# Optimization experiments

Hardware: AMD Instinct MI355X
Metric: run time of the kernel (lower is better)

## Reference

```python
import jax, jax.numpy as jnp
import numpy as np

N, IN, H, C, HID, OUT, E = 4096, 28, 8, 256, 256, 128, 131072
NEG_SLOPE = 0.2


def _gat(x, src, dst, eattr, W, a_src, a_dst, W_e, a_edge, bias, concat):
    # PyG GATConv with edge_dim: add self-loops (edge_attr fill = mean),
    # per-edge attention logits, scatter-softmax over destination nodes.
    n = x.shape[0]
    loop = jnp.arange(n, dtype=src.dtype)
    src = jnp.concatenate([src, loop])
    dst = jnp.concatenate([dst, loop])
    mean_attr = jnp.broadcast_to(eattr.mean(axis=0, keepdims=True), (n, eattr.shape[1]))
    eattr = jnp.concatenate([eattr, mean_attr], axis=0)
    xp = (x @ W).reshape(n, H, C)                       # (N,H,C)
    a_s = (xp * a_src).sum(-1)                          # (N,H)
    a_d = (xp * a_dst).sum(-1)                          # (N,H)
    ep = (eattr @ W_e).reshape(-1, H, C)                # (E',H,C)
    a_e = (ep * a_edge).sum(-1)                         # (E',H)
    alpha = jax.nn.leaky_relu(a_s[src] + a_d[dst] + a_e, negative_slope=NEG_SLOPE)
    mx = jax.ops.segment_max(alpha, dst, num_segments=n)
    ex = jnp.exp(alpha - mx[dst])
    den = jax.ops.segment_sum(ex, dst, num_segments=n)
    w = ex / (den[dst] + 1e-16)                         # (E',H)
    out = jax.ops.segment_sum(xp[src] * w[:, :, None], dst, num_segments=n)  # (N,H,C)
    out = out.reshape(n, H * C) if concat else out.mean(axis=1)
    return out + bias


def _lstm_step(x, W_ih, W_hh, b_ih, b_hh):
    # single-timestep LSTM, zero initial (h, c); torch gate order i,f,g,o
    g = x @ W_ih.T + b_ih + b_hh
    i, f, gg, o = jnp.split(g, 4, axis=-1)
    c = jax.nn.sigmoid(i) * jnp.tanh(gg)
    return jax.nn.sigmoid(o) * jnp.tanh(c)


def _mha(x, in_w, in_b, out_w, out_b, nh):
    n, e = x.shape
    hd = e // nh
    qkv = x @ in_w.T + in_b
    q, k, v = jnp.split(qkv, 3, axis=-1)
    q = q.reshape(n, nh, hd).transpose(1, 0, 2)
    k = k.reshape(n, nh, hd).transpose(1, 0, 2)
    v = v.reshape(n, nh, hd).transpose(1, 0, 2)
    scale = jnp.asarray(1.0 / np.sqrt(hd), x.dtype)
    s = jnp.einsum('hnd,hmd->hnm', q, k) * scale
    p = jax.nn.softmax(s, axis=-1)
    o = jnp.einsum('hnm,hmd->hnd', p, v).transpose(1, 0, 2).reshape(n, e)
    return o @ out_w.T + out_b


def _forward(x, ei_t, ei_c, ea_t, ea_c,
             W_t, a_src_t, a_dst_t, We_t, a_edge_t, b_t,
             W_c, a_src_c, a_dst_c, We_c, a_edge_c, b_c,
             lstm_Wih, lstm_Whh, lstm_bih, lstm_bhh,
             mha_in_w, mha_in_b, mha_out_w, mha_out_b,
             fus_w, fus_b, out_w, out_b):
    # temporal branch: GAT (concat heads) -> 1-step LSTM
    h_t = _gat(x, ei_t[0], ei_t[1], ea_t, W_t, a_src_t, a_dst_t, We_t, a_edge_t, b_t, True)
    h_temporal = _lstm_step(h_t, lstm_Wih, lstm_Whh, lstm_bih, lstm_bhh)   # (N,HID)
    # causal branch: GAT (mean heads -> HID) -> full self-attention over nodes
    h_c = _gat(x, ei_c[0], ei_c[1], ea_c, W_c, a_src_c, a_dst_c, We_c, a_edge_c, b_c, False)
    h_causal = _mha(h_c, mha_in_w, mha_in_b, mha_out_w, mha_out_b, 4)      # (N,HID)
    h = jnp.concatenate([h_temporal, h_causal], axis=-1)
    h = jax.nn.relu(h @ fus_w.T + fus_b)
    out = h @ out_w.T + out_b
    return out, h_temporal, h_causal


def setup_inputs() -> dict:
    key = jax.random.key(0)
    ks = jax.random.split(key, 32)
    s = 0.05
    d = {
        'x': jax.random.normal(ks[0], (N, IN), jnp.float32),
        'edge_index_temporal': jax.random.randint(ks[1], (2, E), 0, N, jnp.int32),
        'edge_index_causal': jax.random.randint(ks[2], (2, E), 0, N, jnp.int32),
        'edge_attr_temporal': jax.random.uniform(ks[3], (E, 1), jnp.float32),
        'edge_attr_causal': jax.random.uniform(ks[4], (E, 1), jnp.float32),
        'W_t': jax.random.normal(ks[5], (IN, H * C), jnp.float32) * s,
        'a_src_t': jax.random.normal(ks[6], (H, C), jnp.float32) * s,
        'a_dst_t': jax.random.normal(ks[7], (H, C), jnp.float32) * s,
        'We_t': jax.random.normal(ks[8], (1, H * C), jnp.float32) * s,
        'a_edge_t': jax.random.normal(ks[9], (H, C), jnp.float32) * s,
        'b_t': jnp.zeros((H * C,), jnp.float32),
        'W_c': jax.random.normal(ks[10], (IN, H * C), jnp.float32) * s,
        'a_src_c': jax.random.normal(ks[11], (H, C), jnp.float32) * s,
        'a_dst_c': jax.random.normal(ks[12], (H, C), jnp.float32) * s,
        'We_c': jax.random.normal(ks[13], (1, H * C), jnp.float32) * s,
        'a_edge_c': jax.random.normal(ks[14], (H, C), jnp.float32) * s,
        'b_c': jnp.zeros((C,), jnp.float32),
        'lstm_Wih': jax.random.normal(ks[15], (4 * HID, H * C), jnp.float32) * s,
        'lstm_Whh': jax.random.normal(ks[16], (4 * HID, HID), jnp.float32) * s,
        'lstm_bih': jnp.zeros((4 * HID,), jnp.float32),
        'lstm_bhh': jnp.zeros((4 * HID,), jnp.float32),
        'mha_in_w': jax.random.normal(ks[17], (3 * HID, HID), jnp.float32) * s,
        'mha_in_b': jnp.zeros((3 * HID,), jnp.float32),
        'mha_out_w': jax.random.normal(ks[18], (HID, HID), jnp.float32) * s,
        'mha_out_b': jnp.zeros((HID,), jnp.float32),
        'fus_w': jax.random.normal(ks[19], (HID, 2 * HID), jnp.float32) * s,
        'fus_b': jnp.zeros((HID,), jnp.float32),
        'out_w': jax.random.normal(ks[20], (OUT, HID), jnp.float32) * s,
        'out_b': jnp.zeros((OUT,), jnp.float32),
    }
    return d


def reference(x, edge_index_temporal, edge_index_causal, edge_attr_temporal, edge_attr_causal,
              W_t, a_src_t, a_dst_t, We_t, a_edge_t, b_t,
              W_c, a_src_c, a_dst_c, We_c, a_edge_c, b_c,
              lstm_Wih, lstm_Whh, lstm_bih, lstm_bhh,
              mha_in_w, mha_in_b, mha_out_w, mha_out_b,
              fus_w, fus_b, out_w, out_b):
    return _forward(x, edge_index_temporal, edge_index_causal, edge_attr_temporal, edge_attr_causal,
                    W_t, a_src_t, a_dst_t, We_t, a_edge_t, b_t,
                    W_c, a_src_c, a_dst_c, We_c, a_edge_c, b_c,
                    lstm_Wih, lstm_Whh, lstm_bih, lstm_bhh,
                    mha_in_w, mha_in_b, mha_out_w, mha_out_b,
                    fus_w, fus_b, out_w, out_b)
```

## Files before the change

kernel.cpp:

```cpp
#include <hip/hip_runtime.h>
#include <hip/hip_bf16.h>

constexpr int NN_ = 4096;
constexpr int INF = 28;
constexpr int NH  = 8;
constexpr int CC  = 256;
constexpr int HC  = 2048;
constexpr int HID = 256;
constexpr int NE  = 131072;
constexpr int KK  = NH * INF;

typedef short bf16x8 __attribute__((ext_vector_type(8)));
typedef short bf16x4 __attribute__((ext_vector_type(4)));
typedef float f32x4 __attribute__((ext_vector_type(4)));

__device__ inline void split_store(float v, __hip_bfloat16* H, __hip_bfloat16* L, size_t idx)
{
    __hip_bfloat16 h = __float2bfloat16(v);
    H[idx] = h;
    L[idx] = __float2bfloat16(v - __bfloat162float(h));
}

__device__ inline short f2bs(float v)
{
    __hip_bfloat16 h = __float2bfloat16(v);
    return *reinterpret_cast<short*>(&h);
}

__device__ inline float wave_sum(float v)
{
    v += __shfl_xor(v, 1);  v += __shfl_xor(v, 2);  v += __shfl_xor(v, 4);
    v += __shfl_xor(v, 8);  v += __shfl_xor(v, 16); v += __shfl_xor(v, 32);
    return v;
}

__global__ void k_stage1(
    const float* __restrict__ Wih,  __hip_bfloat16* WihH,  __hip_bfloat16* WihL,
    const float* __restrict__ Wt,   __hip_bfloat16* WtH,   __hip_bfloat16* WtL,
    const float* __restrict__ minw, __hip_bfloat16* minH,  __hip_bfloat16* minL,
    const float* __restrict__ moutw,__hip_bfloat16* moutH, __hip_bfloat16* moutL,
    const float* __restrict__ fusw, __hip_bfloat16* fusH,  __hip_bfloat16* fusL,
    const float* __restrict__ outw, __hip_bfloat16* outH,  __hip_bfloat16* outL,
    const float* __restrict__ Wc,   __hip_bfloat16* BH,    __hip_bfloat16* BL,
    const float* __restrict__ ast, const float* __restrict__ adt,
    const float* __restrict__ Wet, const float* __restrict__ aet,
    const float* __restrict__ asc, const float* __restrict__ adc,
    const float* __restrict__ Wec, const float* __restrict__ aec,
    float* __restrict__ wa, float* __restrict__ dote,
    const float* __restrict__ bt, const float* __restrict__ bih, const float* __restrict__ bhh,
    float* __restrict__ bg,
    const float* __restrict__ ea_t, const float* __restrict__ ea_c,
    const int* __restrict__ ei_t, const int* __restrict__ ei_c,
    float* __restrict__ meanpart, int* __restrict__ cnt)
{
    int bx = blockIdx.x;
    if (bx < 2576) {
        int i = (bx * 256 + threadIdx.x) * 4;
        if (i < 2580480) {
            const float* src; __hip_bfloat16 *H, *L; int o;
            if (i < 2097152)      { src = Wih;  H = WihH;  L = WihL;  o = i; }
            else if (i < 2154496) { src = Wt;   H = WtH;   L = WtL;   o = i - 2097152; }
            else if (i < 2351104) { src = minw; H = minH;  L = minL;  o = i - 2154496; }
            else if (i < 2416640) { src = moutw;H = moutH; L = moutL; o = i - 2351104; }
            else if (i < 2547712) { src = fusw; H = fusH;  L = fusL;  o = i - 2416640; }
            else                  { src = outw; H = outH;  L = outL;  o = i - 2547712; }
            float4 v = *(const float4*)(src + o);
            short4 hs, ls;
            hs.x = f2bs(v.x); hs.y = f2bs(v.y); hs.z = f2bs(v.z); hs.w = f2bs(v.w);
            __hip_bfloat16* hp = (__hip_bfloat16*)&hs;
            ls.x = f2bs(v.x - __bfloat162float(hp[0]));
            ls.y = f2bs(v.y - __bfloat162float(hp[1]));
            ls.z = f2bs(v.z - __bfloat162float(hp[2]));
            ls.w = f2bs(v.w - __bfloat162float(hp[3]));
            *(short4*)((short*)H + o) = hs;
            *(short4*)((short*)L + o) = ls;
        } else {
            int i2 = i - 2580480;
#pragma unroll
            for (int q = 0; q < 4; ++q) {
                int j = i2 + q;
                int c = j / KK, kk = j % KK;
                int h = kk / INF, k = kk % INF;
                split_store(Wc[k * HC + h * CC + c] * 0.125f, BH, BL, j);
            }
        }
    } else if (bx < 2804) {
        int w = ((bx - 2576) * 256 + threadIdx.x) >> 6;
        int lane = threadIdx.x & 63;
        if (w < 2 * 2 * INF * NH) {
            int b = w / (2 * INF * NH);
            int r = w % (2 * INF * NH);
            int kind = r / (INF * NH);
            int r2 = r % (INF * NH);
            int k = r2 / NH, h = r2 % NH;
            const float* Wm = b ? Wc : Wt;
            const float* a  = b ? (kind ? adc : asc) : (kind ? adt : ast);
            float s = 0.f;
            for (int c = lane; c < CC; c += 64) s += Wm[k * HC + h * CC + c] * a[h * CC + c];
            s = wave_sum(s);
            if (lane == 0) wa[((b * 2 + kind) * INF + k) * NH + h] = s;
        } else if (w < 2 * 2 * INF * NH + 16) {
            int j = w - 2 * 2 * INF * NH;
            int b = j / NH, h = j % NH;
            const float* We = b ? Wec : Wet;
            const float* a  = b ? aec : aet;
            float s = 0.f;
            for (int c = lane; c < CC; c += 64) s += We[h * CC + c] * a[h * CC + c];
            s = wave_sum(s);
            if (lane == 0) dote[b * NH + h] = s;
        }
    } else if (bx < 3060) {
        int j = ((bx - 2804) * 256 + threadIdx.x) >> 6;
        int lane = threadIdx.x & 63;
        if (j < 1024) {
            const float* w = Wih + (size_t)j * HC;
            float s = 0.f;
            for (int c = lane; c < HC; c += 64) s += bt[c] * w[c];
            s = wave_sum(s);
            if (lane == 0) bg[j] = s + bih[j] + bhh[j];
        }
    } else {
        int rel = bx - 3060;
        int i = rel * 256 + threadIdx.x;
        int b = i >> 17, e = i & (NE - 1);
        float v = (b ? ea_c : ea_t)[e];
        for (int off = 32; off; off >>= 1) v += __shfl_down(v, off);
        if ((threadIdx.x & 63) == 0)
            atomicAdd(&meanpart[b * 256 + (rel & 255)], v);
        const int* ei = b ? ei_c : ei_t;
        atomicAdd(&cnt[b * NN_ + ei[NE + e]], 1);
    }
}

__global__ __launch_bounds__(256) void k_stage2(
    const float* __restrict__ x, const float* __restrict__ wa, float* __restrict__ asd,
    const int* __restrict__ cnt, int* __restrict__ rows,
    const float* __restrict__ meanpart, float* __restrict__ meansum)
{
    int bx = blockIdx.x;
    if (bx < 512) {
        int i = bx * 256 + threadIdx.x;
        int bk = i / (NN_ * NH);
        int r = i % (NN_ * NH);
        int n = r / NH, h = r % NH;
        const float* W = wa + bk * INF * NH;
        const float* xr = x + n * INF;
        float s = 0.f;
#pragma unroll
        for (int k = 0; k < INF; ++k) s += xr[k] * W[k * NH + h];
        asd[(bk * NN_ + n) * NH + h] = s;
    } else if (bx < 514) {
        int b = bx - 512;
        const int* c = cnt + b * NN_;
        int* r = rows + b * (NN_ + 16);
        __shared__ int ts[256];
        int t = threadIdx.x;
        int v[16]; int s = 0;
#pragma unroll
        for (int i = 0; i < 16; ++i) { v[i] = c[t * 16 + i]; s += v[i]; }
        ts[t] = s;
        __syncthreads();
        for (int off = 1; off < 256; off <<= 1) {
            int add = (t >= off) ? ts[t - off] : 0;
            __syncthreads();
            ts[t] += add;
            __syncthreads();
        }
        int excl = t ? ts[t - 1] : 0;
#pragma unroll
        for (int i = 0; i < 16; ++i) { r[t * 16 + i] = excl; excl += v[i]; }
        if (t == 255) r[NN_] = excl;
    } else {
        int t = threadIdx.x;
        float v0 = meanpart[t];
        float v1 = meanpart[256 + t];
        v0 = wave_sum(v0);
        v1 = wave_sum(v1);
        __shared__ float s0[4], s1[4];
        if ((t & 63) == 0) { s0[t >> 6] = v0; s1[t >> 6] = v1; }
        __syncthreads();
        if (t == 0) meansum[0] = s0[0] + s0[1] + s0[2] + s0[3];
        if (t == 1) meansum[1] = s1[0] + s1[1] + s1[2] + s1[3];
    }
}

__global__ void k_scatter(const int* __restrict__ ei_t, const int* __restrict__ ei_c,
                          const float* __restrict__ ea_t, const float* __restrict__ ea_c,
                          const int* __restrict__ rows, int* __restrict__ cur,
                          int* __restrict__ srcs, float* __restrict__ eav)
{
    int i = blockIdx.x * blockDim.x + threadIdx.x;
    if (i >= 2 * NE) return;
    int b = i / NE, e = i - b * NE;
    const int* ei = b ? ei_c : ei_t;
    const float* ea = b ? ea_c : ea_t;
    int d = ei[NE + e];
    int pos = rows[b * (NN_ + 16) + d] + atomicAdd(&cur[b * NN_ + d], 1);
    srcs[b * NE + pos] = ei[e];
    eav[b * NE + pos] = ea[e];
}

__global__ __launch_bounds__(64) void k_gat(
    const int* __restrict__ srcs, const float* __restrict__ eav,
    const int* __restrict__ rows, const float* __restrict__ x,
    const float* __restrict__ asd, const float* __restrict__ dote,
    const float* __restrict__ meansum,
    __hip_bfloat16* __restrict__ gH, __hip_bfloat16* __restrict__ gL)
{
    int b = blockIdx.x >> 12;
    int n = blockIdx.x & 4095;
    srcs += (size_t)b * NE; eav += (size_t)b * NE; rows += b * (NN_ + 16);
    const float* a_s = asd + (size_t)(2 * b) * NN_ * NH;
    const float* a_d = asd + (size_t)(2 * b + 1) * NN_ * NH;
    dote += b * NH;
    gH += (size_t)b * NN_ * KK; gL += (size_t)b * NN_ * KK;

    int lane = threadIdx.x;
    __shared__ float xb[64][32];
    __shared__ float eb[64][8];
    __shared__ float denb[8];

    float adn[NH], dt[NH];
#pragma unroll
    for (int h = 0; h < NH; ++h) { adn[h] = a_d[n * NH + h]; dt[h] = dote[h]; }
    float mean_attr = meansum[b] * (1.0f / NE);

    const int hOwn = lane >> 3;
    const int kOwn = (lane & 7) * 4;

    float acc0, acc1, acc2, acc3;
    {
        float al = a_s[n * NH + hOwn] + adn[hOwn] + mean_attr * dt[hOwn];
        al = al > 0.f ? al : 0.2f * al;
        float es = __expf(al);
        float xv0 = (kOwn + 0 < INF) ? x[n * INF + kOwn + 0] : 0.f;
        float xv1 = (kOwn + 1 < INF) ? x[n * INF + kOwn + 1] : 0.f;
        float xv2 = (kOwn + 2 < INF) ? x[n * INF + kOwn + 2] : 0.f;
        float xv3 = (kOwn + 3 < INF) ? x[n * INF + kOwn + 3] : ((kOwn + 3 == 31) ? 1.f : 0.f);
        acc0 = es * xv0; acc1 = es * xv1; acc2 = es * xv2; acc3 = es * xv3;
    }

    int e0 = rows[n], e1 = rows[n + 1];
    for (int base = e0; base < e1; base += 64) {
        int m = e1 - base; if (m > 64) m = 64;
        if (lane < m) {
            int sidx = srcs[base + lane];
            float ea = eav[base + lane];
            const float4* xr = (const float4*)(x + sidx * INF);
#pragma unroll
            for (int q = 0; q < 7; ++q) ((float4*)&xb[lane][0])[q] = xr[q];
            xb[lane][28] = 0.f; xb[lane][29] = 0.f; xb[lane][30] = 0.f; xb[lane][31] = 1.f;
            const float* asr = a_s + sidx * NH;
#pragma unroll
            for (int h = 0; h < NH; ++h) {
                float al = asr[h] + adn[h] + ea * dt[h];
                al = al > 0.f ? al : 0.2f * al;
                eb[lane][h] = __expf(al);
            }
        }
        __syncthreads();
        for (int j = 0; j < m; ++j) {
            float e = eb[j][hOwn];
            float4 xv = *(const float4*)&xb[j][kOwn];
            acc0 += e * xv.x; acc1 += e * xv.y; acc2 += e * xv.z; acc3 += e * xv.w;
        }
        __syncthreads();
    }

    if ((lane & 7) == 7) denb[hOwn] = acc3;
    __syncthreads();
    float inv = 1.0f / denb[hOwn];
    size_t gr = (size_t)n * KK + hOwn * INF + kOwn;
    if (kOwn + 0 < INF) split_store(acc0 * inv, gH, gL, gr + 0);
    if (kOwn + 1 < INF) split_store(acc1 * inv, gH, gL, gr + 1);
    if (kOwn + 2 < INF) split_store(acc2 * inv, gH, gL, gr + 2);
    if (kOwn + 3 < INF) split_store(acc3 * inv, gH, gL, gr + 3);
}

template<bool RELU, int MS, int EPI>
__global__ __launch_bounds__(256) void k_mgemm(
    const __hip_bfloat16* __restrict__ Ahi_, const __hip_bfloat16* __restrict__ Alo_, int lda, int aOffZ,
    const __hip_bfloat16* __restrict__ Bhi_, const __hip_bfloat16* __restrict__ Blo_, int ldb, int bOffZ,
    const float* __restrict__ bias,
    float* __restrict__ Cf, int ldcf,
    __hip_bfloat16* __restrict__ Chi, __hip_bfloat16* __restrict__ Clo, int ldch, int cOffZ,
    __hip_bfloat16* __restrict__ Qbp, __hip_bfloat16* __restrict__ Kbp, __hip_bfloat16* __restrict__ Vtp,
    int M, int N, int K)
{
    int z = blockIdx.z;
    const short* Ah = (const short*)Ahi_ + (size_t)z * aOffZ;
    const short* Al = (const short*)Alo_ + (size_t)z * aOffZ;
    const short* Bh = (const short*)Bhi_ + (size_t)z * bOffZ;
    const short* Bl = (const short*)Blo_ + (size_t)z * bOffZ;
    int wave = threadIdx.x >> 6, lane = threadIdx.x & 63;
    int l16 = lane & 15, lgrp = lane >> 4;
    int m0 = blockIdx.x * (64 * MS) + wave * (16 * MS);
    int n0 = blockIdx.y * 64;

    f32x4 acc[MS][4];
#pragma unroll
    for (int i = 0; i < MS; ++i)
#pragma unroll
        for (int j = 0; j < 4; ++j) acc[i][j] = (f32x4){0.f, 0.f, 0.f, 0.f};

    int nrow[4]; bool nval[4];
#pragma unroll
    for (int ns = 0; ns < 4; ++ns) { nrow[ns] = n0 + ns * 16 + l16; nval[ns] = nrow[ns] < N; }

#pragma unroll 2
    for (int k0 = 0; k0 < K; k0 += 32) {
        size_t ka = (size_t)k0 + lgrp * 8;
        bf16x8 ah[MS], al[MS];
#pragma unroll
        for (int ms = 0; ms < MS; ++ms) {
            ah[ms] = *(const bf16x8*)(Ah + (size_t)(m0 + ms * 16 + l16) * lda + ka);
            al[ms] = *(const bf16x8*)(Al + (size_t)(m0 + ms * 16 + l16) * lda + ka);
        }
        bf16x8 bh[4], bl[4];
#pragma unroll
        for (int ns = 0; ns < 4; ++ns) {
            bh[ns] = (bf16x8){0, 0, 0, 0, 0, 0, 0, 0};
            bl[ns] = (bf16x8){0, 0, 0, 0, 0, 0, 0, 0};
            if (nval[ns]) {
                bh[ns] = *(const bf16x8*)(Bh + (size_t)nrow[ns] * ldb + ka);
                bl[ns] = *(const bf16x8*)(Bl + (size_t)nrow[ns] * ldb + ka);
            }
        }
#pragma unroll
        for (int ns = 0; ns < 4; ++ns)
#pragma unroll
            for (int ms = 0; ms < MS; ++ms) {
                acc[ms][ns] = __builtin_amdgcn_mfma_f32_16x16x32_bf16(ah[ms], bh[ns], acc[ms][ns], 0, 0, 0);
                acc[ms][ns] = __builtin_amdgcn_mfma_f32_16x16x32_bf16(ah[ms], bl[ns], acc[ms][ns], 0, 0, 0);
                acc[ms][ns] = __builtin_amdgcn_mfma_f32_16x16x32_bf16(al[ms], bh[ns], acc[ms][ns], 0, 0, 0);
            }
    }

#pragma unroll
    for (int ms = 0; ms < MS; ++ms)
#pragma unroll
        for (int ns = 0; ns < 4; ++ns)
#pragma unroll
            for (int r = 0; r < 4; ++r) {
                int m = m0 + ms * 16 + lgrp * 4 + r;
                int n = n0 + ns * 16 + l16;
                if (n >= N) continue;
                float v = acc[ms][ns][r];
                if (bias) v += bias[n];
                if (RELU) v = v > 0.f ? v : 0.f;
                if (EPI == 1) {
                    int sec = n >> 8, hh = (n >> 6) & 3, d = n & 63;
                    if (sec == 0)      Qbp[((size_t)hh * NN_ + m) * 64 + d] = __float2bfloat16(v * 0.125f);
                    else if (sec == 1) Kbp[((size_t)hh * NN_ + m) * 64 + d] = __float2bfloat16(v);
                    else {
                        int p = m & 31;
                        int kp = (((p & 15) >> 2) << 3) + ((p >> 4) << 2) + (p & 3);
                        Vtp[(((size_t)hh * (NN_ / 32) + (m >> 5)) * 64 + d) * 32 + kp]
                            = __float2bfloat16(v);
                    }
                } else {
                    if (Cf) Cf[(size_t)m * ldcf + n] = v;
                    if (Chi) split_store(v, Chi, Clo, (size_t)m * ldch + (size_t)z * cOffZ + n);
                }
            }
}

__global__ __launch_bounds__(256) void k_gates_lstm(
    const __hip_bfloat16* __restrict__ gHi, const __hip_bfloat16* __restrict__ gLo,
    const __hip_bfloat16* __restrict__ MtH, const __hip_bfloat16* __restrict__ MtL,
    const float* __restrict__ bg,
    float* __restrict__ hout, __hip_bfloat16* __restrict__ ccH, __hip_bfloat16* __restrict__ ccL)
{
    int wave = threadIdx.x >> 6, lane = threadIdx.x & 63;
    int l16 = lane & 15, lgrp = lane >> 4;
    int m0 = blockIdx.x * 64 + wave * 16;
    int n0 = blockIdx.y * 64;
    const short* Ah = (const short*)gHi;
    const short* Al = (const short*)gLo;
    const short* Bh = (const short*)MtH;
    const short* Bl = (const short*)MtL;

    bf16x8 ah[7], al[7];
#pragma unroll
    for (int k = 0; k < 7; ++k) {
        size_t ka = (size_t)k * 32 + lgrp * 8;
        ah[k] = *(const bf16x8*)(Ah + (size_t)(m0 + l16) * KK + ka);
        al[k] = *(const bf16x8*)(Al + (size_t)(m0 + l16) * KK + ka);
    }

    const int secBase[3] = {0, 512, 768};
    f32x4 acc[3][4];
#pragma unroll
    for (int s = 0; s < 3; ++s) {
#pragma unroll
        for (int ns = 0; ns < 4; ++ns) acc[s][ns] = (f32x4){0.f, 0.f, 0.f, 0.f};
        const short* Bhs = Bh + (size_t)(secBase[s] + n0) * KK;
        const short* Bls = Bl + (size_t)(secBase[s] + n0) * KK;
#pragma unroll
        for (int k = 0; k < 7; ++k) {
            size_t ka = (size_t)k * 32 + lgrp * 8;
            bf16x8 bh[4], bl[4];
#pragma unroll
            for (int ns = 0; ns < 4; ++ns) {
                bh[ns] = *(const bf16x8*)(Bhs + (size_t)(ns * 16 + l16) * KK + ka);
                bl[ns] = *(const bf16x8*)(Bls + (size_t)(ns * 16 + l16) * KK + ka);
            }
#pragma unroll
            for (int ns = 0; ns < 4; ++ns) {
                acc[s][ns] = __builtin_amdgcn_mfma_f32_16x16x32_bf16(ah[k], bh[ns], acc[s][ns], 0, 0, 0);
                acc[s][ns] = __builtin_amdgcn_mfma_f32_16x16x32_bf16(ah[k], bl[ns], acc[s][ns], 0, 0, 0);
                acc[s][ns] = __builtin_amdgcn_mfma_f32_16x16x32_bf16(al[k], bh[ns], acc[s][ns], 0, 0, 0);
            }
        }
    }

#pragma unroll
    for (int ns = 0; ns < 4; ++ns)
#pragma unroll
        for (int r = 0; r < 4; ++r) {
            int m = m0 + lgrp * 4 + r;
            int n = n0 + ns * 16 + l16;
            float gi = acc[0][ns][r] + bg[n];
            float gg = acc[1][ns][r] + bg[512 + n];
            float go = acc[2][ns][r] + bg[768 + n];
            float c = (1.f / (1.f + __expf(-gi))) * tanhf(gg);
            float h = (1.f / (1.f + __expf(-go))) * tanhf(c);
            hout[(size_t)m * 256 + n] = h;
            split_store(h, ccH, ccL, (size_t)m * 512 + n);
        }
}

__global__ __launch_bounds__(512, 2) void k_attn_mfma(
    const __hip_bfloat16* __restrict__ Qb, const __hip_bfloat16* __restrict__ Kb,
    const __hip_bfloat16* __restrict__ Vt,
    __hip_bfloat16* __restrict__ aoH, __hip_bfloat16* __restrict__ aoL)
{
    __shared__ float redN[4][2][16][65];
    __shared__ float redD[4][2][16];
    int tid = threadIdx.x;
    int wave = tid >> 6, lane = tid & 63;
    int l16 = lane & 15, lgrp = lane >> 4;
    int wg = blockIdx.x;
    int xcd = wg & 7;
    int h = xcd >> 1;
    int q0 = (((wg >> 3) << 1) | (xcd & 1)) * 32;
    int kbase = wave * 512;

    const short* Qs = (const short*)Qb;
    const short* Kbase_ = (const short*)Kb + (size_t)h * NN_ * 64;
    const short* Vbase_ = (const short*)Vt + (size_t)h * NN_ * 64;

    bf16x8 qf[2][2];
#pragma unroll
    for (int qt = 0; qt < 2; ++qt)
#pragma unroll
        for (int dh = 0; dh < 2; ++dh)
            qf[qt][dh] = *(const bf16x8*)(Qs + ((size_t)h * NN_ + q0 + qt * 16 + l16) * 64 + dh * 32 + lgrp * 8);

    f32x4 oacc[2][4];
#pragma unroll
    for (int qt = 0; qt < 2; ++qt)
#pragma unroll
        for (int dc = 0; dc < 4; ++dc) oacc[qt][dc] = (f32x4){0.f, 0.f, 0.f, 0.f};
    float dn[2] = {0.f, 0.f};

    bf16x8 kA[2][2], kB[2][2];
    bf16x8 vA[4], vB[4];

#define LOADK(K0, kf)                                                                 \
    { int k0_ = (K0);                                                                 \
      _Pragma("unroll") for (int kh = 0; kh < 2; ++kh)                                \
      _Pragma("unroll") for (int dh = 0; dh < 2; ++dh)                                \
          kf[kh][dh] = *(const bf16x8*)(Kbase_ + (size_t)(k0_ + kh * 16 + l16) * 64   \
                                        + dh * 32 + lgrp * 8); }
#define LOADV(K0, vf)                                                                 \
    { const short* tb_ = Vbase_ + ((size_t)((K0) >> 5)) * 2048;                       \
      _Pragma("unroll") for (int dc = 0; dc < 4; ++dc)                                \
          vf[dc] = *(const bf16x8*)(tb_ + (dc * 16 + l16) * 32 + lgrp * 8); }
#define COMPUTE(kf, vf)                                                               \
    { f32x4 st_[2][2];                                                                \
      _Pragma("unroll") for (int kh = 0; kh < 2; ++kh)                                \
      _Pragma("unroll") for (int qt = 0; qt < 2; ++qt) {                              \
          f32x4 s_ = (f32x4){0.f, 0.f, 0.f, 0.f};                                     \
          s_ = __builtin_amdgcn_mfma_f32_16x16x32_bf16(kf[kh][0], qf[qt][0], s_, 0, 0, 0); \
          s_ = __builtin_amdgcn_mfma_f32_16x16x32_bf16(kf[kh][1], qf[qt][1], s_, 0, 0, 0); \
          st_[kh][qt] = s_; }                                                         \
      _Pragma("unroll") for (int qt = 0; qt < 2; ++qt) {                              \
          bf16x8 pa_;                                                                 \
          float dsum_ = 0.f;                                                          \
          _Pragma("unroll") for (int r = 0; r < 4; ++r) {                             \
              float e0_ = __expf(st_[0][qt][r]);                                      \
              float e1_ = __expf(st_[1][qt][r]);                                      \
              dsum_ += e0_ + e1_;                                                     \
              pa_[r]     = f2bs(e0_);                                                 \
              pa_[4 + r] = f2bs(e1_); }                                               \
          dn[qt] += dsum_;                                                            \
          _Pragma("unroll") for (int dc = 0; dc < 4; ++dc)                            \
              oacc[qt][dc] = __builtin_amdgcn_mfma_f32_16x16x32_bf16(pa_, vf[dc], oacc[qt][dc], 0, 0, 0); } }

    LOADK(kbase, kA); LOADV(kbase, vA);
    for (int kt = 0; kt < 16; kt += 2) {
        int k1 = kbase + (kt + 1) * 32;
        LOADK(k1, kB); LOADV(k1, vB);
        COMPUTE(kA, vA);
        if (kt + 2 < 16) {
            int k2 = kbase + (kt + 2) * 32;
            LOADK(k2, kA); LOADV(k2, vA);
        }
        COMPUTE(kB, vB);
    }
#undef LOADK
#undef LOADV
#undef COMPUTE

#pragma unroll
    for (int qt = 0; qt < 2; ++qt) {
        dn[qt] += __shfl_xor(dn[qt], 16);
        dn[qt] += __shfl_xor(dn[qt], 32);
    }

#define STORE_(s)                                                                   \
    {                                                                               \
        _Pragma("unroll") for (int qt = 0; qt < 2; ++qt) {                          \
            _Pragma("unroll") for (int dc = 0; dc < 4; ++dc)                        \
                _Pragma("unroll") for (int r = 0; r < 4; ++r)                       \
                    redN[s][qt][lgrp * 4 + r][dc * 16 + l16] = oacc[qt][dc][r];     \
            if (lane < 16) redD[s][qt][lane] = dn[qt];                              \
        }                                                                           \
    }
#define ACCUM_(s)                                                                   \
    {                                                                               \
        _Pragma("unroll") for (int qt = 0; qt < 2; ++qt) {                          \
            _Pragma("unroll") for (int dc = 0; dc < 4; ++dc)                        \
                _Pragma("unroll") for (int r = 0; r < 4; ++r)                       \
                    oacc[qt][dc][r] += redN[s][qt][lgrp * 4 + r][dc * 16 + l16];    \
            dn[qt] += redD[s][qt][l16];                                             \
        }                                                                           \
    }
    if (wave >= 4) STORE_(wave - 4);
    __syncthreads();
    if (wave < 4) ACCUM_(wave);
    __syncthreads();
    if (wave == 2 || wave == 3) STORE_(wave - 2);
    __syncthreads();
    if (wave < 2) ACCUM_(wave);
    __syncthreads();
    if (wave == 1) STORE_(0);
    __syncthreads();
    if (wave == 0) {
        ACCUM_(0);
#pragma unroll
        for (int qt = 0; qt < 2; ++qt) {
            float inv = 1.f / dn[qt];
#pragma unroll
            for (int r = 0; r < 4; ++r) {
                float invr = __shfl(inv, lgrp * 4 + r);
#pragma unroll
                for (int dc = 0; dc < 4; ++dc)
                    split_store(oacc[qt][dc][r] * invr, aoH, aoL,
                                (size_t)(q0 + qt * 16 + lgrp * 4 + r) * 256 + h * 64 + dc * 16 + l16);
            }
        }
    }
#undef STORE_
#undef ACCUM_
}

extern "C" void kernel_launch(void* const* d_in, const int* in_sizes, int n_in,
                              void* d_out, int out_size, void* d_ws, size_t ws_size,
                              hipStream_t stream)
{
    const float* x      = (const float*)d_in[0];
    const int*   ei_t   = (const int*)d_in[1];
    const int*   ei_c   = (const int*)d_in[2];
    const float* ea_t   = (const float*)d_in[3];
    const float* ea_c   = (const float*)d_in[4];
    const float* W_t    = (const float*)d_in[5];
    const float* asrc_t = (const float*)d_in[6];
    const float* adst_t = (const float*)d_in[7];
    const float* We_t   = (const float*)d_in[8];
    const float* aedg_t = (const float*)d_in[9];
    const float* b_t    = (const float*)d_in[10];
    const float* W_c    = (const float*)d_in[11];
    const float* asrc_c = (const float*)d_in[12];
    const float* adst_c = (const float*)d_in[13];
    const float* We_c   = (const float*)d_in[14];
    const float* aedg_c = (const float*)d_in[15];
    const float* b_c    = (const float*)d_in[16];
    const float* Wih    = (const float*)d_in[17];
    const float* bih    = (const float*)d_in[19];
    const float* bhh    = (const float*)d_in[20];
    const float* min_w  = (const float*)d_in[21];
    const float* min_b  = (const float*)d_in[22];
    const float* mout_w = (const float*)d_in[23];
    const float* mout_b = (const float*)d_in[24];
    const float* fus_w  = (const float*)d_in[25];
    const float* fus_b  = (const float*)d_in[26];
    const float* out_w  = (const float*)d_in[27];
    const float* out_b  = (const float*)d_in[28];
    float* outp = (float*)d_out;

    char* W = (char*)d_ws;
    size_t off = 0;
    auto alloc = [&](size_t bytes) { size_t r = off; off += (bytes + 255) & ~(size_t)255; return r; };
    size_t oMeanPart = alloc(512 * 4);
    size_t oCnt   = alloc(2 * NN_ * 4);
    size_t oCur   = alloc(2 * NN_ * 4);
    size_t zeroBytes = off;
    size_t oMean  = alloc(2 * 4);
    size_t oRows  = alloc(2 * (NN_ + 16) * 4);
    size_t oSrcs  = alloc(2 * NE * 4);
    size_t oEav   = alloc(2 * NE * 4);
    size_t oWa    = alloc(4 * INF * NH * 4);
    size_t oDote  = alloc(2 * NH * 4);
    size_t oAsd   = alloc(4 * NN_ * NH * 4);
    size_t oBg    = alloc(1024 * 4);
    size_t oGH    = alloc((size_t)2 * NN_ * KK * 2);
    size_t oGL    = alloc((size_t)2 * NN_ * KK * 2);
    size_t oMtH   = alloc((size_t)1024 * KK * 2);
    size_t oMtL   = alloc((size_t)1024 * KK * 2);
    size_t oBctH  = alloc((size_t)CC * KK * 2);
    size_t oBctL  = alloc((size_t)CC * KK * 2);
    size_t oWihH  = alloc((size_t)1024 * HC * 2);
    size_t oWihL  = alloc((size_t)1024 * HC * 2);
    size_t oWtH   = alloc((size_t)INF * HC * 2);
    size_t oWtL   = alloc((size_t)INF * HC * 2);
    size_t oMinH  = alloc((size_t)768 * HID * 2);
    size_t oMinL  = alloc((size_t)768 * HID * 2);
    size_t oMoutH = alloc((size_t)HID * HID * 2);
    size_t oMoutL = alloc((size_t)HID * HID * 2);
    size_t oFusH  = alloc((size_t)HID * 512 * 2);
    size_t oFusL  = alloc((size_t)HID * 512 * 2);
    size_t oOutwH = alloc((size_t)128 * HID * 2);
    size_t oOutwL = alloc((size_t)128 * HID * 2);
    size_t oHcH   = alloc((size_t)NN_ * HID * 2);
    size_t oHcL   = alloc((size_t)NN_ * HID * 2);
    size_t oQb    = alloc((size_t)4 * NN_ * 64 * 2);
    size_t oKb    = alloc((size_t)4 * NN_ * 64 * 2);
    size_t oVt    = alloc((size_t)4 * NN_ * 64 * 2);
    size_t oCcH   = oWihH;
    size_t oCcL   = oWihL;
    size_t oAoH   = oGH;
    size_t oAoL   = oGL;
    size_t oHfH   = oHcH;
    size_t oHfL   = oHcL;
    (void)ws_size; (void)in_sizes; (void)n_in; (void)out_size;

    hipMemsetAsync(W, 0, zeroBytes, stream);

    k_stage1<<<4084, 256, 0, stream>>>(
        Wih,    (__hip_bfloat16*)(W + oWihH),  (__hip_bfloat16*)(W + oWihL),
        W_t,    (__hip_bfloat16*)(W + oWtH),   (__hip_bfloat16*)(W + oWtL),
        min_w,  (__hip_bfloat16*)(W + oMinH),  (__hip_bfloat16*)(W + oMinL),
        mout_w, (__hip_bfloat16*)(W + oMoutH), (__hip_bfloat16*)(W + oMoutL),
        fus_w,  (__hip_bfloat16*)(W + oFusH),  (__hip_bfloat16*)(W + oFusL),
        out_w,  (__hip_bfloat16*)(W + oOutwH), (__hip_bfloat16*)(W + oOutwL),
        W_c,    (__hip_bfloat16*)(W + oBctH),  (__hip_bfloat16*)(W + oBctL),
        asrc_t, adst_t, We_t, aedg_t, asrc_c, adst_c, We_c, aedg_c,
        (float*)(W + oWa), (float*)(W + oDote),
        b_t, bih, bhh, (float*)(W + oBg),
        ea_t, ea_c, ei_t, ei_c, (float*)(W + oMeanPart), (int*)(W + oCnt));
    k_stage2<<<515, 256, 0, stream>>>(x, (float*)(W + oWa), (float*)(W + oAsd),
                                      (int*)(W + oCnt), (int*)(W + oRows),
                                      (float*)(W + oMeanPart), (float*)(W + oMean));
    {
        dim3 grid(8, 1, 8);
        k_mgemm<false, 2, 0><<<grid, 256, 0, stream>>>(
            (__hip_bfloat16*)(W + oWihH), (__hip_bfloat16*)(W + oWihL), HC, CC,
            (__hip_bfloat16*)(W + oWtH),  (__hip_bfloat16*)(W + oWtL),  HC, CC,
            nullptr, nullptr, 0,
            (__hip_bfloat16*)(W + oMtH), (__hip_bfloat16*)(W + oMtL), KK, INF,
            nullptr, nullptr, nullptr,
            1024, INF, CC);
    }
    k_scatter<<<2 * NE / 256, 256, 0, stream>>>(ei_t, ei_c, ea_t, ea_c,
                                                (int*)(W + oRows), (int*)(W + oCur),
                                                (int*)(W + oSrcs), (float*)(W + oEav));
    k_gat<<<2 * NN_, 64, 0, stream>>>((int*)(W + oSrcs), (float*)(W + oEav), (int*)(W + oRows), x,
                                      (float*)(W + oAsd), (float*)(W + oDote), (float*)(W + oMean),
                                      (__hip_bfloat16*)(W + oGH), (__hip_bfloat16*)(W + oGL));
    {
        dim3 grid(NN_ / 64, HID / 64);
        k_gates_lstm<<<grid, 256, 0, stream>>>(
            (__hip_bfloat16*)(W + oGH), (__hip_bfloat16*)(W + oGL),
            (__hip_bfloat16*)(W + oMtH), (__hip_bfloat16*)(W + oMtL),
            (float*)(W + oBg),
            outp + 524288, (__hip_bfloat16*)(W + oCcH), (__hip_bfloat16*)(W + oCcL));
    }
    {
        dim3 grid(64, 4, 1);
        k_mgemm<false, 1, 0><<<grid, 256, 0, stream>>>(
            (__hip_bfloat16*)(W + oGH) + (size_t)NN_ * KK, (__hip_bfloat16*)(W + oGL) + (size_t)NN_ * KK, KK, 0,
            (__hip_bfloat16*)(W + oBctH), (__hip_bfloat16*)(W + oBctL), KK, 0,
            b_c, nullptr, 0,
            (__hip_bfloat16*)(W + oHcH), (__hip_bfloat16*)(W + oHcL), HID, 0,
            nullptr, nullptr, nullptr,
            NN_, HID, KK);
    }
    {
        dim3 grid(32, 12, 1);
        k_mgemm<false, 2, 1><<<grid, 256, 0, stream>>>(
            (__hip_bfloat16*)(W + oHcH), (__hip_bfloat16*)(W + oHcL), HID, 0,
            (__hip_bfloat16*)(W + oMinH), (__hip_bfloat16*)(W + oMinL), HID, 0,
            min_b, nullptr, 0,
            nullptr, nullptr, 0, 0,
            (__hip_bfloat16*)(W + oQb), (__hip_bfloat16*)(W + oKb), (__hip_bfloat16*)(W + oVt),
            NN_, 768, HID);
    }
    {
        k_attn_mfma<<<512, 512, 0, stream>>>(
            (__hip_bfloat16*)(W + oQb), (__hip_bfloat16*)(W + oKb), (__hip_bfloat16*)(W + oVt),
            (__hip_bfloat16*)(W + oAoH), (__hip_bfloat16*)(W + oAoL));
    }
    {
        dim3 grid(64, 4, 1);
        k_mgemm<false, 1, 0><<<grid, 256, 0, stream>>>(
            (__hip_bfloat16*)(W + oAoH), (__hip_bfloat16*)(W + oAoL), HID, 0,
            (__hip_bfloat16*)(W + oMoutH), (__hip_bfloat16*)(W + oMoutL), HID, 0,
            mout_b, outp + 524288 + 1048576, 256,
            (__hip_bfloat16*)(W + oCcH) + 256, (__hip_bfloat16*)(W + oCcL) + 256, 512, 0,
            nullptr, nullptr, nullptr,
            NN_, HID, HID);
    }
    {
        dim3 grid(64, 4, 1);
        k_mgemm<true, 1, 0><<<grid, 256, 0, stream>>>(
            (__hip_bfloat16*)(W + oCcH), (__hip_bfloat16*)(W + oCcL), 512, 0,
            (__hip_bfloat16*)(W + oFusH), (__hip_bfloat16*)(W + oFusL), 512, 0,
            fus_b, nullptr, 0,
            (__hip_bfloat16*)(W + oHfH), (__hip_bfloat16*)(W + oHfL), HID, 0,
            nullptr, nullptr, nullptr,
            NN_, HID, 512);
    }
    {
        dim3 grid(64, 2, 1);
        k_mgemm<false, 1, 0><<<grid, 256, 0, stream>>>(
            (__hip_bfloat16*)(W + oHfH), (__hip_bfloat16*)(W + oHfL), HID, 0,
            (__hip_bfloat16*)(W + oOutwH), (__hip_bfloat16*)(W + oOutwL), HID, 0,
            out_b, outp, 128,
            nullptr, nullptr, 0, 0,
            nullptr, nullptr, nullptr,
            NN_, 128, HID);
    }
}
```

Measured before the change: 359.2 us.

## Stage GEMM B tiles and attention K/V via global_load_lds with swizzled LDS

The split-bf16 GEMM and gates-LSTM kernels now load each 64x32 B tile cooperatively into LDS with direct global-to-LDS loads and an XOR swizzle, so the four waves share it instead of each fetching it from global memory. The attention kernel moves from 512 to 256 threads per block, with each wave covering twice as many keys and staging its K and V tiles through per-wave LDS buffers. The cross-wave reduction tree loses one level. In exchange, every k-step adds two block barriers, the attention loop no longer double-buffers its register loads, and the GEMM's N-bounds check on B rows is removed.

```diff
diff --git a/kernel.cpp b/kernel.cpp
--- a/kernel.cpp
+++ b/kernel.cpp
@@ -11,7 +11,6 @@
 constexpr int KK  = NH * INF;
 
 typedef short bf16x8 __attribute__((ext_vector_type(8)));
-typedef short bf16x4 __attribute__((ext_vector_type(4)));
 typedef float f32x4 __attribute__((ext_vector_type(4)));
 
 __device__ inline void split_store(float v, __hip_bfloat16* H, __hip_bfloat16* L, size_t idx)
@@ -32,6 +31,13 @@
     v += __shfl_xor(v, 1);  v += __shfl_xor(v, 2);  v += __shfl_xor(v, 4);
     v += __shfl_xor(v, 8);  v += __shfl_xor(v, 16); v += __shfl_xor(v, 32);
     return v;
+}
+
+__device__ inline void load_lds16(const void* g, void* l)
+{
+    __builtin_amdgcn_global_load_lds(
+        (const __attribute__((address_space(1))) void*)g,
+        (__attribute__((address_space(3))) void*)l, 16, 0, 0);
 }
 
 __global__ void k_stage1(
@@ -287,6 +293,7 @@
     __hip_bfloat16* __restrict__ Qbp, __hip_bfloat16* __restrict__ Kbp, __hip_bfloat16* __restrict__ Vtp,
     int M, int N, int K)
 {
+    __shared__ short bstage[4096];
     int z = blockIdx.z;
     const short* Ah = (const short*)Ahi_ + (size_t)z * aOffZ;
     const short* Al = (const short*)Alo_ + (size_t)z * aOffZ;
@@ -303,28 +310,39 @@
 #pragma unroll
         for (int j = 0; j < 4; ++j) acc[i][j] = (f32x4){0.f, 0.f, 0.f, 0.f};
 
-    int nrow[4]; bool nval[4];
-#pragma unroll
-    for (int ns = 0; ns < 4; ++ns) { nrow[ns] = n0 + ns * 16 + l16; nval[ns] = nrow[ns] < N; }
-
-#pragma unroll 2
+    int gsrc[2], cc_[2]; bool hi_[2];
+#pragma unroll
+    for (int j = 0; j < 2; ++j) {
+        int c = wave * 2 + j;
+        hi_[j] = c < 4; cc_[j] = c & 3;
+        int w = cc_[j] * 64 + lane;
+        gsrc[j] = w ^ ((w >> 2) & 3);
+    }
+
     for (int k0 = 0; k0 < K; k0 += 32) {
-        size_t ka = (size_t)k0 + lgrp * 8;
+#pragma unroll
+        for (int j = 0; j < 2; ++j) {
+            const short* src = hi_[j] ? Bh : Bl;
+            int g = gsrc[j];
+            load_lds16(src + (size_t)(n0 + (g >> 2)) * ldb + k0 + (g & 3) * 8,
+                       &bstage[(hi_[j] ? 0 : 2048) + cc_[j] * 512]);
+        }
+        __syncthreads();
+
         bf16x8 ah[MS], al[MS];
 #pragma unroll
         for (int ms = 0; ms < MS; ++ms) {
+            size_t ka = (size_t)k0 + lgrp * 8;
             ah[ms] = *(const bf16x8*)(Ah + (size_t)(m0 + ms * 16 + l16) * lda + ka);
             al[ms] = *(const bf16x8*)(Al + (size_t)(m0 + ms * 16 + l16) * lda + ka);
         }
         bf16x8 bh[4], bl[4];
 #pragma unroll
         for (int ns = 0; ns < 4; ++ns) {
-            bh[ns] = (bf16x8){0, 0, 0, 0, 0, 0, 0, 0};
-            bl[ns] = (bf16x8){0, 0, 0, 0, 0, 0, 0, 0};
-            if (nval[ns]) {
-                bh[ns] = *(const bf16x8*)(Bh + (size_t)nrow[ns] * ldb + ka);
-                bl[ns] = *(const bf16x8*)(Bl + (size_t)nrow[ns] * ldb + ka);
-            }
+            int u = (ns * 16 + l16) * 4 + lgrp;
+            int us = u ^ (l16 & 3);
+            bh[ns] = *(const bf16x8*)&bstage[us * 8];
+            bl[ns] = *(const bf16x8*)&bstage[2048 + us * 8];
         }
 #pragma unroll
         for (int ns = 0; ns < 4; ++ns)
@@ -334,6 +352,7 @@
                 acc[ms][ns] = __builtin_amdgcn_mfma_f32_16x16x32_bf16(ah[ms], bl[ns], acc[ms][ns], 0, 0, 0);
                 acc[ms][ns] = __builtin_amdgcn_mfma_f32_16x16x32_bf16(al[ms], bh[ns], acc[ms][ns], 0, 0, 0);
             }
+        __syncthreads();
     }
 
 #pragma unroll
@@ -371,6 +390,7 @@
     const float* __restrict__ bg,
     float* __restrict__ hout, __hip_bfloat16* __restrict__ ccH, __hip_bfloat16* __restrict__ ccL)
 {
+    __shared__ short bstage[4096];
     int wave = threadIdx.x >> 6, lane = threadIdx.x & 63;
     int l16 = lane & 15, lgrp = lane >> 4;
     int m0 = blockIdx.x * 64 + wave * 16;
@@ -388,22 +408,41 @@
         al[k] = *(const bf16x8*)(Al + (size_t)(m0 + l16) * KK + ka);
     }
 
+    int gsrc[2], cc_[2]; bool hi_[2];
+#pragma unroll
+    for (int j = 0; j < 2; ++j) {
+        int c = wave * 2 + j;
+        hi_[j] = c < 4; cc_[j] = c & 3;
+        int w = cc_[j] * 64 + lane;
+        gsrc[j] = w ^ ((w >> 2) & 3);
+    }
+
     const int secBase[3] = {0, 512, 768};
     f32x4 acc[3][4];
 #pragma unroll
+    for (int s = 0; s < 3; ++s)
+#pragma unroll
+        for (int ns = 0; ns < 4; ++ns) acc[s][ns] = (f32x4){0.f, 0.f, 0.f, 0.f};
+
     for (int s = 0; s < 3; ++s) {
-#pragma unroll
-        for (int ns = 0; ns < 4; ++ns) acc[s][ns] = (f32x4){0.f, 0.f, 0.f, 0.f};
-        const short* Bhs = Bh + (size_t)(secBase[s] + n0) * KK;
-        const short* Bls = Bl + (size_t)(secBase[s] + n0) * KK;
-#pragma unroll
+        int rbase = secBase[s] + n0;
         for (int k = 0; k < 7; ++k) {
-            size_t ka = (size_t)k * 32 + lgrp * 8;
+            int k0 = k * 32;
+#pragma unroll
+            for (int j = 0; j < 2; ++j) {
+                const short* src = hi_[j] ? Bh : Bl;
+                int g = gsrc[j];
+                load_lds16(src + (size_t)(rbase + (g >> 2)) * KK + k0 + (g & 3) * 8,
+                           &bstage[(hi_[j] ? 0 : 2048) + cc_[j] * 512]);
+            }
+            __syncthreads();
             bf16x8 bh[4], bl[4];
 #pragma unroll
             for (int ns = 0; ns < 4; ++ns) {
-                bh[ns] = *(const bf16x8*)(Bhs + (size_t)(ns * 16 + l16) * KK + ka);
-                bl[ns] = *(const bf16x8*)(Bls + (size_t)(ns * 16 + l16) * KK + ka);
+                int u = (ns * 16 + l16) * 4 + lgrp;
+                int us = u ^ (l16 & 3);
+                bh[ns] = *(const bf16x8*)&bstage[us * 8];
+                bl[ns] = *(const bf16x8*)&bstage[2048 + us * 8];
             }
 #pragma unroll
             for (int ns = 0; ns < 4; ++ns) {
@@ -411,6 +450,7 @@
                 acc[s][ns] = __builtin_amdgcn_mfma_f32_16x16x32_bf16(ah[k], bl[ns], acc[s][ns], 0, 0, 0);
                 acc[s][ns] = __builtin_amdgcn_mfma_f32_16x16x32_bf16(al[k], bh[ns], acc[s][ns], 0, 0, 0);
             }
+            __syncthreads();
         }
     }
 
@@ -430,13 +470,15 @@
         }
 }
 
-__global__ __launch_bounds__(512, 2) void k_attn_mfma(
+__global__ __launch_bounds__(256) void k_attn_mfma(
     const __hip_bfloat16* __restrict__ Qb, const __hip_bfloat16* __restrict__ Kb,
     const __hip_bfloat16* __restrict__ Vt,
     __hip_bfloat16* __restrict__ aoH, __hip_bfloat16* __restrict__ aoL)
 {
-    __shared__ float redN[4][2][16][65];
-    __shared__ float redD[4][2][16];
+    __shared__ short kst[4][2048];
+    __shared__ short vst[4][2048];
+    __shared__ float redN[2][2][16][65];
+    __shared__ float redD[2][2][16];
     int tid = threadIdx.x;
     int wave = tid >> 6, lane = tid & 63;
     int l16 = lane & 15, lgrp = lane >> 4;
@@ -444,11 +486,11 @@
     int xcd = wg & 7;
     int h = xcd >> 1;
     int q0 = (((wg >> 3) << 1) | (xcd & 1)) * 32;
-    int kbase = wave * 512;
+    int kbase = wave * 1024;
 
     const short* Qs = (const short*)Qb;
-    const short* Kbase_ = (const short*)Kb + (size_t)h * NN_ * 64;
-    const short* Vbase_ = (const short*)Vt + (size_t)h * NN_ * 64;
+    const short* Kg = (const short*)Kb + (size_t)h * NN_ * 64;
+    const short* Vg = (const short*)Vt + (size_t)h * NN_ * 64;
 
     bf16x8 qf[2][2];
 #pragma unroll
@@ -464,54 +506,69 @@
         for (int dc = 0; dc < 4; ++dc) oacc[qt][dc] = (f32x4){0.f, 0.f, 0.f, 0.f};
     float dn[2] = {0.f, 0.f};
 
-    bf16x8 kA[2][2], kB[2][2];
-    bf16x8 vA[4], vB[4];
-
-#define LOADK(K0, kf)                                                                 \
-    { int k0_ = (K0);                                                                 \
-      _Pragma("unroll") for (int kh = 0; kh < 2; ++kh)                                \
-      _Pragma("unroll") for (int dh = 0; dh < 2; ++dh)                                \
-          kf[kh][dh] = *(const bf16x8*)(Kbase_ + (size_t)(k0_ + kh * 16 + l16) * 64   \
-                                        + dh * 32 + lgrp * 8); }
-#define LOADV(K0, vf)                                                                 \
-    { const short* tb_ = Vbase_ + ((size_t)((K0) >> 5)) * 2048;                       \
-      _Pragma("unroll") for (int dc = 0; dc < 4; ++dc)                                \
-          vf[dc] = *(const bf16x8*)(tb_ + (dc * 16 + l16) * 32 + lgrp * 8); }
-#define COMPUTE(kf, vf)                                                               \
-    { f32x4 st_[2][2];                                                                \
-      _Pragma("unroll") for (int kh = 0; kh < 2; ++kh)                                \
-      _Pragma("unroll") for (int qt = 0; qt < 2; ++qt) {                              \
-          f32x4 s_ = (f32x4){0.f, 0.f, 0.f, 0.f};                                     \
-          s_ = __builtin_amdgcn_mfma_f32_16x16x32_bf16(kf[kh][0], qf[qt][0], s_, 0, 0, 0); \
-          s_ = __builtin_amdgcn_mfma_f32_16x16x32_bf16(kf[kh][1], qf[qt][1], s_, 0, 0, 0); \
-          st_[kh][qt] = s_; }                                                         \
-      _Pragma("unroll") for (int qt = 0; qt < 2; ++qt) {                              \
-          bf16x8 pa_;                                                                 \
-          float dsum_ = 0.f;                                                          \
-          _Pragma("unroll") for (int r = 0; r < 4; ++r) {                             \
-              float e0_ = __expf(st_[0][qt][r]);                                      \
-              float e1_ = __expf(st_[1][qt][r]);                                      \
-              dsum_ += e0_ + e1_;                                                     \
-              pa_[r]     = f2bs(e0_);                                                 \
-              pa_[4 + r] = f2bs(e1_); }                                               \
-          dn[qt] += dsum_;                                                            \
-          _Pragma("unroll") for (int dc = 0; dc < 4; ++dc)                            \
-              oacc[qt][dc] = __builtin_amdgcn_mfma_f32_16x16x32_bf16(pa_, vf[dc], oacc[qt][dc], 0, 0, 0); } }
-
-    LOADK(kbase, kA); LOADV(kbase, vA);
-    for (int kt = 0; kt < 16; kt += 2) {
-        int k1 = kbase + (kt + 1) * 32;
-        LOADK(k1, kB); LOADV(k1, vB);
-        COMPUTE(kA, vA);
-        if (kt + 2 < 16) {
-            int k2 = kbase + (kt + 2) * 32;
-            LOADK(k2, kA); LOADV(k2, vA);
-        }
-        COMPUTE(kB, vB);
-    }
-#undef LOADK
-#undef LOADV
-#undef COMPUTE
+    int gk[4], gv[4];
+#pragma unroll
+    for (int c = 0; c < 4; ++c) {
+        int w = c * 64 + lane;
+        gk[c] = w ^ ((w >> 3) & 7);
+        gv[c] = w ^ ((w >> 2) & 3);
+    }
+
+    for (int kt = 0; kt < 32; ++kt) {
+        int k0 = kbase + kt * 32;
+        const short* ktile = Kg + (size_t)k0 * 64;
+        const short* vtile = Vg + (size_t)(k0 >> 5) * 2048;
+#pragma unroll
+        for (int c = 0; c < 4; ++c)
+            load_lds16(ktile + (size_t)(gk[c] >> 3) * 64 + (gk[c] & 7) * 8, &kst[wave][c * 512]);
+#pragma unroll
+        for (int c = 0; c < 4; ++c)
+            load_lds16(vtile + (gv[c] >> 2) * 32 + (gv[c] & 3) * 8, &vst[wave][c * 512]);
+        asm volatile("s_waitcnt vmcnt(0)" ::: "memory");
+
+        bf16x8 kf[2][2], vf[4];
+#pragma unroll
+        for (int kh = 0; kh < 2; ++kh)
+#pragma unroll
+            for (int dh = 0; dh < 2; ++dh) {
+                int u = (kh * 16 + l16) * 8 + dh * 4 + lgrp;
+                kf[kh][dh] = *(const bf16x8*)&kst[wave][(u ^ (l16 & 7)) * 8];
+            }
+#pragma unroll
+        for (int dc = 0; dc < 4; ++dc) {
+            int u = (dc * 16 + l16) * 4 + lgrp;
+            vf[dc] = *(const bf16x8*)&vst[wave][(u ^ (l16 & 3)) * 8];
+        }
+
+        f32x4 st[2][2];
+#pragma unroll
+        for (int kh = 0; kh < 2; ++kh)
+#pragma unroll
+            for (int qt = 0; qt < 2; ++qt) {
+                f32x4 s = (f32x4){0.f, 0.f, 0.f, 0.f};
+                s = __builtin_amdgcn_mfma_f32_16x16x32_bf16(kf[kh][0], qf[qt][0], s, 0, 0, 0);
+                s = __builtin_amdgcn_mfma_f32_16x16x32_bf16(kf[kh][1], qf[qt][1], s, 0, 0, 0);
+                st[kh][qt] = s;
+            }
+#pragma unroll
+        for (int qt = 0; qt < 2; ++qt) {
+            bf16x8 pa;
+            float dsum = 0.f;
+#pragma unroll
+            for (int r = 0; r < 4; ++r) {
+                float e0 = __expf(st[0][qt][r]);
+                float e1 = __expf(st[1][qt][r]);
+                dsum += e0 + e1;
+                pa[r]     = f2bs(e0);
+                pa[4 + r] = f2bs(e1);
+            }
+            dn[qt] += dsum;
+#pragma unroll
+            for (int dc = 0; dc < 4; ++dc)
+                oacc[qt][dc] = __builtin_amdgcn_mfma_f32_16x16x32_bf16(pa, vf[dc], oacc[qt][dc], 0, 0, 0);
+        }
+        asm volatile("s_waitcnt lgkmcnt(0)" ::: "memory");
+    }
 
 #pragma unroll
     for (int qt = 0; qt < 2; ++qt) {
@@ -537,11 +594,7 @@
             dn[qt] += redD[s][qt][l16];                                             \
         }                                                                           \
     }
-    if (wave >= 4) STORE_(wave - 4);
-    __syncthreads();
-    if (wave < 4) ACCUM_(wave);
-    __syncthreads();
-    if (wave == 2 || wave == 3) STORE_(wave - 2);
+    if (wave >= 2) STORE_(wave - 2);
     __syncthreads();
     if (wave < 2) ACCUM_(wave);
     __syncthreads();
@@ -708,7 +761,7 @@
             NN_, 768, HID);
     }
     {
-        k_attn_mfma<<<512, 512, 0, stream>>>(
+        k_attn_mfma<<<512, 256, 0, stream>>>(
             (__hip_bfloat16*)(W + oQb), (__hip_bfloat16*)(W + oKb), (__hip_bfloat16*)(W + oVt),
             (__hip_bfloat16*)(W + oAoH), (__hip_bfloat16*)(W + oAoL));
     }
```

New measurement: 318.0 us. 1.13x faster.
